# Kernel tuning notes

Measured on AMD Instinct MI355X. Metric: run time of the kernel, lower is better.

## Reference

```python
import jax, jax.numpy as jnp
import numpy as np

N_DATA = 128      # number of datasets (process conditions)
SEG_LEN = 131072  # thickness points per dataset
N_MAT = 8         # number of distinct materials
N_MATP = 8        # material params: Sigma0, BetaD, Ea, Mfda, Di, A0, B0, l0
N_PROCP = 5       # process params: SigmaC, K0, alpha1, L0, GrainSize_200
RGAS = 8.314      # gas constant, J/(mol K)


def setup_inputs() -> dict:
    key = jax.random.key(0)
    k1, k2, k3, k4 = jax.random.split(key, 4)
    # thickness points: sorted within each dataset segment, scaled to [0, 1]
    x = jax.random.uniform(k1, (N_DATA, SEG_LEN), dtype=jnp.float32)
    x_scaled = jnp.sort(x, axis=1).reshape(-1)
    # process conditions [R, T, P, Melting_T]
    pc = jax.random.uniform(k2, (N_DATA, 4), dtype=jnp.float32)
    R = 0.05 + pc[:, 0]            # deposition rate
    T = 300.0 + 300.0 * pc[:, 1]   # temperature (K)
    P = 0.1 + pc[:, 2]             # pressure
    material_index = jnp.sort(jax.random.randint(k3, (N_DATA,), 0, N_MAT, dtype=jnp.int32))
    melting_T = 1000.0 + 100.0 * material_index.astype(jnp.float32)
    process_c = jnp.stack([R, T, P, melting_T], axis=1)
    # learned raw parameters (pre-sigmoid) and bounds
    n_params = N_MAT * N_MATP + N_DATA * N_PROCP  # 704
    raw_params = 0.5 * jax.random.normal(k4, (n_params,), dtype=jnp.float32)
    para_lb = jnp.full((n_params,), 0.1, dtype=jnp.float32)
    para_ub = jnp.full((n_params,), 2.0, dtype=jnp.float32)
    # MinMaxScaler surrogates: [x_data_min, x_data_max, y_data_min, y_data_max], feature_range=(0,1)
    scaler_params = jnp.array([0.5, 500.0, -50.0, 50.0], dtype=jnp.float32)
    fit_index = jnp.repeat(jnp.arange(1, N_DATA + 1, dtype=jnp.int32), SEG_LEN)
    return {
        'x_scaled': x_scaled, 'process_c': process_c, 'raw_params': raw_params,
        'para_lb': para_lb, 'para_ub': para_ub, 'scaler_params': scaler_params,
        'fit_index': fit_index, 'material_index': material_index,
    }


def _stress(tp, R, T, P, SigmaC, alpha1, L0, G200, Sigma0, BetaD, Ea, Mfda, Di, A0, B0, l0):
    """Kinetic stress equation (Chason-type). tp: [N, L-1]; params broadcast [N, 1]."""
    Lg = G200 * (tp / 200.0 + 1e-3) ** alpha1 + L0      # grain size evolution
    D = Di * jnp.exp(-Ea / (RGAS * T))                   # thermally activated diffusivity
    beta = BetaD * D / (R * Lg + 1e-9)                   # kinetic competition factor
    sigma_ss = (SigmaC - Mfda * P + (Sigma0 / Lg) * beta) / (1.0 + beta)
    return sigma_ss + A0 * jnp.exp(-tp / (B0 * l0 + 1e-9))  # steady-state + transient


def reference(x_scaled, process_c, raw_params, para_lb, para_ub, scaler_params,
              fit_index, material_index):
    n_data = process_c.shape[0]
    seg = x_scaled.shape[0] // n_data
    # unscale parameters: sigmoid -> [lb, ub]
    xv = jax.nn.sigmoid(raw_params) * (para_ub - para_lb) + para_lb
    materials = xv[:N_MAT * N_MATP].reshape(N_MAT, N_MATP)
    process = xv[N_MAT * N_MATP:].reshape(n_data, N_PROCP)
    x_min, x_max, y_min, y_max = scaler_params[0], scaler_params[1], scaler_params[2], scaler_params[3]
    # inverse MinMax transform of thickness (feature_range = (0, 1))
    t = (x_scaled * (x_max - x_min) + x_min).reshape(n_data, seg)  # [N, L]
    SigmaC, K0, alpha1, L0, G200 = (process[:, i:i + 1] for i in range(5))
    mat = materials[material_index]  # [N, 8] gather per-dataset material params
    Sigma0, BetaD, Ea, Mfda, Di, A0, B0, l0 = (mat[:, i:i + 1] for i in range(8))
    R, T, P = process_c[:, 0:1], process_c[:, 1:2], process_c[:, 2:3]
    # Euler integration: Fit[j+1] = Fit[j] + stress(t[j]) * dT  ==  K0 + cumsum
    s = _stress(t[:, :-1], R, T, P, SigmaC, alpha1, L0, G200,
                Sigma0, BetaD, Ea, Mfda, Di, A0, B0, l0)   # [N, L-1]
    dT = jnp.diff(t, axis=1)                                # [N, L-1]
    fit = jnp.concatenate([K0, K0 + jnp.cumsum(s * dT, axis=1)], axis=1).reshape(-1)
    # forward MinMax transform of stress-thickness (feature_range = (0, 1))
    return (fit - y_min) / (y_max - y_min)
```

## Files before the change

kernel.cpp:

```cpp
#include <hip/hip_runtime.h>

#define N_DATA   128
#define SEG_LEN  131072
#define NPROD    (SEG_LEN - 1)
#define N_MAT    8
#define N_MATP   8
#define N_PROCP  5
#define RGAS     8.314f

#define TPB      1024
#define EPT      8
#define TILE     (TPB * EPT)
#define NITER    (SEG_LEN / TILE)
#define NWAVE    (TPB / 64)

__device__ __forceinline__ float stress_s(float t,
    float alpha1, float L0, float G200, float Sigma0, float A0,
    float inv_tau, float cbd, float base_num, float R) {
  float Lg  = G200 * __expf(alpha1 * __logf(t * (1.0f / 200.0f) + 0.001f)) + L0;
  float u   = R * Lg + 1e-9f;
  float num = base_num * u * Lg + Sigma0 * cbd;
  float den = Lg * (u + cbd);
  float sigma_ss = num * __builtin_amdgcn_rcpf(den);
  return sigma_ss + A0 * __expf(-t * inv_tau);
}

__global__ __launch_bounds__(TPB) void row_scan(
    const float* __restrict__ x,
    const float* __restrict__ pc,
    const float* __restrict__ raw,
    const float* __restrict__ lb,
    const float* __restrict__ ub,
    const float* __restrict__ sc,
    const int*  __restrict__ mat_idx,
    float* __restrict__ out) {
  __shared__ float rc[16];
  __shared__ float wtot[2][NWAVE];

  int row = blockIdx.x;
  int tid = threadIdx.x;

  if (tid == 0) {
    auto xv = [&](int i) {
      float s = 1.0f / (1.0f + __expf(-raw[i]));
      return s * (ub[i] - lb[i]) + lb[i];
    };
    int pb = N_MAT * N_MATP + row * N_PROCP;
    float SigmaC = xv(pb + 0), K0 = xv(pb + 1), alpha1 = xv(pb + 2);
    float L0 = xv(pb + 3), G200 = xv(pb + 4);
    int mb = mat_idx[row] * N_MATP;
    float Sigma0 = xv(mb + 0), BetaD = xv(mb + 1), Ea = xv(mb + 2), Mfda = xv(mb + 3);
    float Di = xv(mb + 4), A0 = xv(mb + 5), B0 = xv(mb + 6), l0 = xv(mb + 7);
    float R = pc[row * 4 + 0], T = pc[row * 4 + 1], P = pc[row * 4 + 2];
    rc[0] = alpha1; rc[1] = L0; rc[2] = G200; rc[3] = Sigma0;
    rc[4] = A0;     rc[5] = 1.0f / (B0 * l0 + 1e-9f);
    rc[6] = BetaD * Di * __expf(-Ea / (RGAS * T));
    rc[7] = SigmaC - Mfda * P;
    rc[8] = R;      rc[9] = K0;
    rc[10] = sc[0]; rc[11] = sc[1] - sc[0];
    rc[12] = sc[2]; rc[13] = 1.0f / (sc[3] - sc[2]);
  }
  __syncthreads();
  float alpha1 = rc[0], L0 = rc[1], G200 = rc[2], Sigma0 = rc[3], A0 = rc[4];
  float inv_tau = rc[5], cbd = rc[6], base_num = rc[7], R = rc[8], K0 = rc[9];
  float x_min = rc[10], x_sc = rc[11], y_min = rc[12], inv_yr = rc[13];

  int lane = tid & 63, wv = tid >> 6;
  long rowbase = (long)row * SEG_LEN;
  const float* xr = x + rowbase;
  float* outr = out + rowbase;

  float carry = K0;

  int gb0 = tid * EPT;
  float4 a  = *(const float4*)(xr + gb0);
  float4 bq = *(const float4*)(xr + gb0 + 4);
  float  xn = xr[gb0 + EPT];

  for (int it = 0; it < NITER; ++it) {
    int gb = it * TILE + tid * EPT;

    float tv[9];
    tv[0] = a.x  * x_sc + x_min; tv[1] = a.y  * x_sc + x_min;
    tv[2] = a.z  * x_sc + x_min; tv[3] = a.w  * x_sc + x_min;
    tv[4] = bq.x * x_sc + x_min; tv[5] = bq.y * x_sc + x_min;
    tv[6] = bq.z * x_sc + x_min; tv[7] = bq.w * x_sc + x_min;
    tv[8] = xn   * x_sc + x_min;

    float4 na, nb; float nxn = 0.0f;
    if (it + 1 < NITER) {
      int ngb = (it + 1) * TILE + tid * EPT;
      na  = *(const float4*)(xr + ngb);
      nb  = *(const float4*)(xr + ngb + 4);
      nxn = (ngb + EPT < SEG_LEN) ? xr[ngb + EPT] : 0.0f;
    }

    float pref[EPT];
    float run = 0.0f;
#pragma unroll
    for (int k = 0; k < EPT; k++) {
      float p = 0.0f;
      if (gb + k < NPROD) {
        float s = stress_s(tv[k], alpha1, L0, G200, Sigma0, A0, inv_tau, cbd, base_num, R);
        p = s * (tv[k + 1] - tv[k]);
      }
      run += p;
      pref[k] = run;
    }

    float incl = run;
#pragma unroll
    for (int d = 1; d < 64; d <<= 1) {
      float n = __shfl_up(incl, d);
      if (lane >= d) incl += n;
    }
    int buf = it & 1;
    if (lane == 63) wtot[buf][wv] = incl;
    __syncthreads();

    float low = 0.0f, tot = 0.0f;
#pragma unroll
    for (int w = 0; w < NWAVE; w++) {
      float v = wtot[buf][w];
      tot += v;
      low += (w < wv) ? v : 0.0f;
    }

    float base = carry + (incl - run) + low;
    carry += tot;

    float4 o0, o1;
    o0.x = (base           - y_min) * inv_yr;
    o0.y = (base + pref[0] - y_min) * inv_yr;
    o0.z = (base + pref[1] - y_min) * inv_yr;
    o0.w = (base + pref[2] - y_min) * inv_yr;
    o1.x = (base + pref[3] - y_min) * inv_yr;
    o1.y = (base + pref[4] - y_min) * inv_yr;
    o1.z = (base + pref[5] - y_min) * inv_yr;
    o1.w = (base + pref[6] - y_min) * inv_yr;
    *(float4*)(outr + gb)     = o0;
    *(float4*)(outr + gb + 4) = o1;

    a = na; bq = nb; xn = nxn;
  }
}

extern "C" void kernel_launch(void* const* d_in, const int* in_sizes, int n_in,
                              void* d_out, int out_size, void* d_ws, size_t ws_size,
                              hipStream_t stream) {
  const float* x_scaled  = (const float*)d_in[0];
  const float* process_c = (const float*)d_in[1];
  const float* raw       = (const float*)d_in[2];
  const float* lb        = (const float*)d_in[3];
  const float* ub        = (const float*)d_in[4];
  const float* sc        = (const float*)d_in[5];
  const int*   mat_idx   = (const int*)d_in[7];
  float* out = (float*)d_out;

  row_scan<<<N_DATA, TPB, 0, stream>>>(
      x_scaled, process_c, raw, lb, ub, sc, mat_idx, out);
}
```

Measured before the change: 201.8 us.

## Split row scan into chunked compute kernel plus carry fixup kernel

Replaces the one-block-per-row sequential scan (128 blocks of 1024 threads looping 16 tiles) with 8192 blocks that each scan a 2048-element chunk independently and write chunk totals to workspace. A second kernel scans the 64 chunk totals per row and adds each chunk's offset to the already-written outputs. This fills far more of the GPU than 128 blocks can, at the cost of an extra full read and write pass over the 64 MB output and a second launch.

Measured after the change: 180.5 us. -10.5%, faster.

```diff
diff --git a/kernel.cpp b/kernel.cpp
--- a/kernel.cpp
+++ b/kernel.cpp
@@ -8,11 +8,10 @@
 #define N_PROCP  5
 #define RGAS     8.314f
 
-#define TPB      1024
+#define NCH      64
+#define CHUNK    2048
+#define TPB      256
 #define EPT      8
-#define TILE     (TPB * EPT)
-#define NITER    (SEG_LEN / TILE)
-#define NWAVE    (TPB / 64)
 
 __device__ __forceinline__ float stress_s(float t,
     float alpha1, float L0, float G200, float Sigma0, float A0,
@@ -25,124 +24,126 @@
   return sigma_ss + A0 * __expf(-t * inv_tau);
 }
 
-__global__ __launch_bounds__(TPB) void row_scan(
+__global__ __launch_bounds__(TPB) void k1_compute(
     const float* __restrict__ x,
-    const float* __restrict__ pc,
-    const float* __restrict__ raw,
-    const float* __restrict__ lb,
-    const float* __restrict__ ub,
-    const float* __restrict__ sc,
-    const int*  __restrict__ mat_idx,
+    const float* __restrict__ pc, const float* __restrict__ raw,
+    const float* __restrict__ lb, const float* __restrict__ ub,
+    const float* __restrict__ sc, const int* __restrict__ mat_idx,
+    float* __restrict__ chunksum_s,
     float* __restrict__ out) {
-  __shared__ float rc[16];
-  __shared__ float wtot[2][NWAVE];
+  __shared__ float pv[13];
+  __shared__ float ws4[4];
 
-  int row = blockIdx.x;
+  int b   = blockIdx.x;
+  int row = b >> 6;
+  int ch  = b & (NCH - 1);
   int tid = threadIdx.x;
+  int lane = tid & 63, wv = tid >> 6;
 
-  if (tid == 0) {
-    auto xv = [&](int i) {
-      float s = 1.0f / (1.0f + __expf(-raw[i]));
-      return s * (ub[i] - lb[i]) + lb[i];
-    };
-    int pb = N_MAT * N_MATP + row * N_PROCP;
-    float SigmaC = xv(pb + 0), K0 = xv(pb + 1), alpha1 = xv(pb + 2);
-    float L0 = xv(pb + 3), G200 = xv(pb + 4);
-    int mb = mat_idx[row] * N_MATP;
-    float Sigma0 = xv(mb + 0), BetaD = xv(mb + 1), Ea = xv(mb + 2), Mfda = xv(mb + 3);
-    float Di = xv(mb + 4), A0 = xv(mb + 5), B0 = xv(mb + 6), l0 = xv(mb + 7);
-    float R = pc[row * 4 + 0], T = pc[row * 4 + 1], P = pc[row * 4 + 2];
-    rc[0] = alpha1; rc[1] = L0; rc[2] = G200; rc[3] = Sigma0;
-    rc[4] = A0;     rc[5] = 1.0f / (B0 * l0 + 1e-9f);
-    rc[6] = BetaD * Di * __expf(-Ea / (RGAS * T));
-    rc[7] = SigmaC - Mfda * P;
-    rc[8] = R;      rc[9] = K0;
-    rc[10] = sc[0]; rc[11] = sc[1] - sc[0];
-    rc[12] = sc[2]; rc[13] = 1.0f / (sc[3] - sc[2]);
+  long rowbase = (long)row * SEG_LEN;
+  int  gb = ch * CHUNK + tid * EPT;
+  const float* xp = x + rowbase + gb;
+  float4 a  = *(const float4*)xp;
+  float4 bq = *(const float4*)(xp + 4);
+  float  xn = (gb + EPT < SEG_LEN) ? xp[EPT] : 0.0f;
+
+  if (tid < 13) {
+    int idx = (tid < 5) ? (N_MAT * N_MATP + row * N_PROCP + tid)
+                        : (mat_idx[row] * N_MATP + (tid - 5));
+    float s = 1.0f / (1.0f + __expf(-raw[idx]));
+    pv[tid] = s * (ub[idx] - lb[idx]) + lb[idx];
   }
   __syncthreads();
-  float alpha1 = rc[0], L0 = rc[1], G200 = rc[2], Sigma0 = rc[3], A0 = rc[4];
-  float inv_tau = rc[5], cbd = rc[6], base_num = rc[7], R = rc[8], K0 = rc[9];
-  float x_min = rc[10], x_sc = rc[11], y_min = rc[12], inv_yr = rc[13];
 
-  int lane = tid & 63, wv = tid >> 6;
-  long rowbase = (long)row * SEG_LEN;
-  const float* xr = x + rowbase;
-  float* outr = out + rowbase;
+  float SigmaC = pv[0], K0 = pv[1], alpha1 = pv[2], L0 = pv[3], G200 = pv[4];
+  float Sigma0 = pv[5], BetaD = pv[6], Ea = pv[7], Mfda = pv[8], Di = pv[9];
+  float A0 = pv[10], B0 = pv[11], l0 = pv[12];
+  float R = pc[row * 4 + 0], T = pc[row * 4 + 1], P = pc[row * 4 + 2];
+  float cbd      = BetaD * Di * __expf(-Ea / (RGAS * T));
+  float base_num = SigmaC - Mfda * P;
+  float inv_tau  = 1.0f / (B0 * l0 + 1e-9f);
+  float x_min = sc[0], x_sc = sc[1] - sc[0];
+  float y_min = sc[2], inv_yr = 1.0f / (sc[3] - sc[2]);
 
-  float carry = K0;
+  float tv[9];
+  tv[0] = a.x  * x_sc + x_min; tv[1] = a.y  * x_sc + x_min;
+  tv[2] = a.z  * x_sc + x_min; tv[3] = a.w  * x_sc + x_min;
+  tv[4] = bq.x * x_sc + x_min; tv[5] = bq.y * x_sc + x_min;
+  tv[6] = bq.z * x_sc + x_min; tv[7] = bq.w * x_sc + x_min;
+  tv[8] = xn   * x_sc + x_min;
 
-  int gb0 = tid * EPT;
-  float4 a  = *(const float4*)(xr + gb0);
-  float4 bq = *(const float4*)(xr + gb0 + 4);
-  float  xn = xr[gb0 + EPT];
+  float pref[EPT];
+  float run = 0.0f;
+#pragma unroll
+  for (int k = 0; k < EPT; k++) {
+    float p = 0.0f;
+    if (gb + k < NPROD) {
+      float s = stress_s(tv[k], alpha1, L0, G200, Sigma0, A0, inv_tau, cbd, base_num, R);
+      p = s * (tv[k + 1] - tv[k]);
+    }
+    run += p;
+    pref[k] = run;
+  }
 
-  for (int it = 0; it < NITER; ++it) {
-    int gb = it * TILE + tid * EPT;
+  float incl = run;
+#pragma unroll
+  for (int d = 1; d < 64; d <<= 1) {
+    float n = __shfl_up(incl, d);
+    if (lane >= d) incl += n;
+  }
+  if (lane == 63) ws4[wv] = incl;
+  __syncthreads();
+  float low = 0.0f, tot = 0.0f;
+#pragma unroll
+  for (int w = 0; w < 4; w++) {
+    float v = ws4[w];
+    tot += v;
+    low += (w < wv) ? v : 0.0f;
+  }
+  float texcl = (incl - run) + low;
 
-    float tv[9];
-    tv[0] = a.x  * x_sc + x_min; tv[1] = a.y  * x_sc + x_min;
-    tv[2] = a.z  * x_sc + x_min; tv[3] = a.w  * x_sc + x_min;
-    tv[4] = bq.x * x_sc + x_min; tv[5] = bq.y * x_sc + x_min;
-    tv[6] = bq.z * x_sc + x_min; tv[7] = bq.w * x_sc + x_min;
-    tv[8] = xn   * x_sc + x_min;
+  if (tid == 0) chunksum_s[b] = tot * inv_yr;
 
-    float4 na, nb; float nxn = 0.0f;
-    if (it + 1 < NITER) {
-      int ngb = (it + 1) * TILE + tid * EPT;
-      na  = *(const float4*)(xr + ngb);
-      nb  = *(const float4*)(xr + ngb + 4);
-      nxn = (ngb + EPT < SEG_LEN) ? xr[ngb + EPT] : 0.0f;
-    }
+  float base = K0 + texcl;
+  float4 o0, o1;
+  o0.x = (base           - y_min) * inv_yr;
+  o0.y = (base + pref[0] - y_min) * inv_yr;
+  o0.z = (base + pref[1] - y_min) * inv_yr;
+  o0.w = (base + pref[2] - y_min) * inv_yr;
+  o1.x = (base + pref[3] - y_min) * inv_yr;
+  o1.y = (base + pref[4] - y_min) * inv_yr;
+  o1.z = (base + pref[5] - y_min) * inv_yr;
+  o1.w = (base + pref[6] - y_min) * inv_yr;
+  float* op = out + rowbase + gb;
+  *(float4*)op       = o0;
+  *(float4*)(op + 4) = o1;
+}
 
-    float pref[EPT];
-    float run = 0.0f;
+__global__ __launch_bounds__(TPB) void k2_fixup(
+    const float* __restrict__ chunksum_s,
+    float* __restrict__ out) {
+  int b   = blockIdx.x;
+  int row = b >> 6;
+  int ch  = b & (NCH - 1);
+  int tid = threadIdx.x;
+  int lane = tid & 63;
+
+  float v = chunksum_s[(row << 6) | lane];
+  float incl = v;
 #pragma unroll
-    for (int k = 0; k < EPT; k++) {
-      float p = 0.0f;
-      if (gb + k < NPROD) {
-        float s = stress_s(tv[k], alpha1, L0, G200, Sigma0, A0, inv_tau, cbd, base_num, R);
-        p = s * (tv[k + 1] - tv[k]);
-      }
-      run += p;
-      pref[k] = run;
-    }
+  for (int d = 1; d < 64; d <<= 1) {
+    float n = __shfl_up(incl, d);
+    if (lane >= d) incl += n;
+  }
+  float add = __shfl(incl - v, ch);
 
-    float incl = run;
-#pragma unroll
-    for (int d = 1; d < 64; d <<= 1) {
-      float n = __shfl_up(incl, d);
-      if (lane >= d) incl += n;
-    }
-    int buf = it & 1;
-    if (lane == 63) wtot[buf][wv] = incl;
-    __syncthreads();
-
-    float low = 0.0f, tot = 0.0f;
-#pragma unroll
-    for (int w = 0; w < NWAVE; w++) {
-      float v = wtot[buf][w];
-      tot += v;
-      low += (w < wv) ? v : 0.0f;
-    }
-
-    float base = carry + (incl - run) + low;
-    carry += tot;
-
-    float4 o0, o1;
-    o0.x = (base           - y_min) * inv_yr;
-    o0.y = (base + pref[0] - y_min) * inv_yr;
-    o0.z = (base + pref[1] - y_min) * inv_yr;
-    o0.w = (base + pref[2] - y_min) * inv_yr;
-    o1.x = (base + pref[3] - y_min) * inv_yr;
-    o1.y = (base + pref[4] - y_min) * inv_yr;
-    o1.z = (base + pref[5] - y_min) * inv_yr;
-    o1.w = (base + pref[6] - y_min) * inv_yr;
-    *(float4*)(outr + gb)     = o0;
-    *(float4*)(outr + gb + 4) = o1;
-
-    a = na; bq = nb; xn = nxn;
-  }
+  long base = (long)row * SEG_LEN + ch * CHUNK + tid * EPT;
+  float4 o0 = *(float4*)(out + base);
+  float4 o1 = *(float4*)(out + base + 4);
+  o0.x += add; o0.y += add; o0.z += add; o0.w += add;
+  o1.x += add; o1.y += add; o1.z += add; o1.w += add;
+  *(float4*)(out + base)     = o0;
+  *(float4*)(out + base + 4) = o1;
 }
 
 extern "C" void kernel_launch(void* const* d_in, const int* in_sizes, int n_in,
@@ -156,7 +157,9 @@
   const float* sc        = (const float*)d_in[5];
   const int*   mat_idx   = (const int*)d_in[7];
   float* out = (float*)d_out;
+  float* chunksum_s = (float*)d_ws;
 
-  row_scan<<<N_DATA, TPB, 0, stream>>>(
-      x_scaled, process_c, raw, lb, ub, sc, mat_idx, out);
+  k1_compute<<<N_DATA * NCH, TPB, 0, stream>>>(
+      x_scaled, process_c, raw, lb, ub, sc, mat_idx, chunksum_s, out);
+  k2_fixup<<<N_DATA * NCH, TPB, 0, stream>>>(chunksum_s, out);
 }
```
